# Performance work log

Hardware: AMD Instinct MI355X
Metric: run time of the kernel (lower is better)

Reference implementation:

```python
import jax, jax.numpy as jnp
import numpy as np

# Analytic closed form of the 4-qubit circuit. Wires (0,1) and (2,3) are
# independent 2-qubit blocks: RY(x_a)oRY(x_b) -> CNOT(a,b) -> RY(p_a)oRY(p_b).
# Heisenberg picture gives:
#   <Z_a> = cos(p_a)*cos(x_a) + sin(p_a)*sin(x_a)*sin(x_b)
#   <Z_b> = cos(p_b)*cos(x_a)*cos(x_b) + sin(p_b)*sin(x_b)

def setup_inputs() -> dict:
    key = jax.random.key(0)
    k1, k2, k3, k4 = jax.random.split(key, 4)
    B = 16384
    return {
        "x": jax.random.uniform(k1, (B, 1, 28, 28), dtype=jnp.float32),
        "vqc_params": jax.random.normal(k2, (4,), dtype=jnp.float32),
        "fc_w": jax.random.normal(k3, (10, 784), dtype=jnp.float32) * 0.05,
        "fc_b": jax.random.normal(k4, (10,), dtype=jnp.float32) * 0.05,
        "bias": jnp.zeros((10,), dtype=jnp.float32),
    }


def _pair_expvals(xa, xb, pa, pb):
    # xa, xb: [B, 196]; pa, pb: scalars
    za = jnp.cos(pa) * jnp.cos(xa) + jnp.sin(pa) * jnp.sin(xa) * jnp.sin(xb)
    zb = jnp.cos(pb) * jnp.cos(xa) * jnp.cos(xb) + jnp.sin(pb) * jnp.sin(xb)
    return za, zb


def reference(x, vqc_params, fc_w, fc_b, bias):
    B = x.shape[0]
    # Extract 2x2 patches in the same (r, c) row-major order as the torch loop.
    # [B,28,28] -> [B,14,2,14,2] -> [B,14,14,2,2] -> [B,196,4]
    p = x[:, 0].reshape(B, 14, 2, 14, 2).transpose(0, 1, 3, 2, 4).reshape(B, 196, 4)
    x0, x1, x2, x3 = p[..., 0], p[..., 1], p[..., 2], p[..., 3]
    p0, p1, p2, p3 = vqc_params[0], vqc_params[1], vqc_params[2], vqc_params[3]
    z0, z1 = _pair_expvals(x0, x1, p0, p1)
    z2, z3 = _pair_expvals(x2, x3, p2, p3)
    q = jnp.stack([z0, z1, z2, z3], axis=-1).reshape(B, 4 * 196)  # patch-major, wire-minor
    logits = q @ fc_w.T + fc_b - bias
    return jax.nn.log_softmax(logits, axis=-1)
```

## Files before the change

kernel.cpp:

```cpp
#include <hip/hip_runtime.h>


typedef __attribute__((ext_vector_type(8))) short short8;
typedef __attribute__((ext_vector_type(4))) float f32x4;

constexpr int WAVES = 4;
constexpr int BLOCK = WAVES * 64;
constexpr int IMGS  = 16;
constexpr int NITER = 7;
constexpr int S2    = 800;

static __device__ __forceinline__ unsigned pkbf2(float lo, float hi) {
    unsigned r;
    asm("v_cvt_pk_bf16_f32 %0, %1, %2" : "=v"(r) : "v"(lo), "v"(hi));
    return r;
}

__global__ __launch_bounds__(BLOCK, 4)
void quanv_mfma(const float* __restrict__ x,
                const float* __restrict__ vqc,
                const float* __restrict__ fc_w,
                const float* __restrict__ fc_b,
                const float* __restrict__ bias,
                float* __restrict__ out,
                int B)
{
    __shared__ __align__(16) unsigned short q_lds[IMGS * S2];
    __shared__ float cpart[3][64 * 4];

    const int tid  = threadIdx.x;
    const int lane = tid & 63;
    const int wv   = tid >> 6;
    const int i16  = lane & 15;
    const int g    = lane >> 4;
    const int imgBase = blockIdx.x * IMGS;

    float S0, C0, S1, C1, S2p, C2p, S3, C3;
    __sincosf(vqc[0], &S0, &C0);
    __sincosf(vqc[1], &S1, &C1);
    __sincosf(vqc[2], &S2p, &C2p);
    __sincosf(vqc[3], &S3, &C3);

    const float4* __restrict__ xf4 =
        reinterpret_cast<const float4*>(x) + (long)imgBase * 196;
    #pragma unroll
    for (int it = 0; it < 13; ++it) {
        const unsigned u = it * BLOCK + tid;
        if (it < 12 || u < 3136u) {
            const float4 v = xf4[u];
            const unsigned img = u / 196u;
            const unsigned jv  = u - 196u * img;
            const unsigned y   = jv / 7u;
            const unsigned cx  = jv - 7u * y;
            const unsigned par = y & 1u;

            const float CA = par ? C2p : C0, SA = par ? S2p : S0;
            const float CB = par ? C3  : C1, SB = par ? S3  : S1;

            float sa, ca, sb, cb;
            __sincosf(v.x, &sa, &ca);  __sincosf(v.y, &sb, &cb);
            const float za1 = CA * ca + SA * (sa * sb);
            const float zb1 = CB * (ca * cb) + SB * sb;
            __sincosf(v.z, &sa, &ca);  __sincosf(v.w, &sb, &cb);
            const float za2 = CA * ca + SA * (sa * sb);
            const float zb2 = CB * (ca * cb) + SB * sb;

            const unsigned qb = ((y >> 1) * 14u + 2u * cx) * 4u + 2u * par;
            const unsigned e  = img * S2 + qb;
            *reinterpret_cast<unsigned*>(&q_lds[e])     = pkbf2(za1, zb1);
            *reinterpret_cast<unsigned*>(&q_lds[e + 4]) = pkbf2(za2, zb2);
        }
    }
    if (tid < 128) {
        const int img = tid >> 3, o = (tid & 7) << 1;
        *reinterpret_cast<unsigned*>(&q_lds[img * S2 + 784 + o]) = 0u;
    }

    const int ncl = (i16 < 10) ? i16 : 9;
    const float* __restrict__ wrow = fc_w + ncl * 784;
    short8 bf[NITER];
    #pragma unroll
    for (int I = 0; I < NITER; ++I) {
        int kb = wv + 4 * I; if (kb > 24) kb = 24;
        int k  = kb * 32 + 8 * g; if (k > 776) k = 776;
        const float4 lo4 = *reinterpret_cast<const float4*>(wrow + k);
        const float4 hi4 = *reinterpret_cast<const float4*>(wrow + k + 4);
        union { unsigned u[4]; short8 s; } t;
        t.u[0] = pkbf2(lo4.x, lo4.y);
        t.u[1] = pkbf2(lo4.z, lo4.w);
        t.u[2] = pkbf2(hi4.x, hi4.y);
        t.u[3] = pkbf2(hi4.z, hi4.w);
        bf[I] = t.s;
    }

    __syncthreads();

    f32x4 acc = {0.f, 0.f, 0.f, 0.f};
    #pragma unroll
    for (int I = 0; I < NITER; ++I) {
        const int kb = wv + 4 * I;
        if (kb < 25) {
            const short8 a = *reinterpret_cast<const short8*>(
                &q_lds[i16 * S2 + kb * 32 + 8 * g]);
            acc = __builtin_amdgcn_mfma_f32_16x16x32_bf16(a, bf[I], acc, 0, 0, 0);
        }
    }

    if (wv > 0)
        *reinterpret_cast<f32x4*>(&cpart[wv - 1][lane * 4]) = acc;
    __syncthreads();

    if (wv == 0) {
        #pragma unroll
        for (int p = 0; p < 3; ++p)
            acc += *reinterpret_cast<const f32x4*>(&cpart[p][lane * 4]);
        const float bk = (i16 < 10) ? (fc_b[i16] - bias[i16]) : 0.f;

        #pragma unroll
        for (int r = 0; r < 4; ++r) {
            const float lg = acc[r] + bk;
            float mx = (i16 < 10) ? lg : -3.0e38f;
            #pragma unroll
            for (int off = 1; off < 16; off <<= 1)
                mx = fmaxf(mx, __shfl_xor(mx, off, 64));
            float s = (i16 < 10) ? __expf(lg - mx) : 0.f;
            #pragma unroll
            for (int off = 1; off < 16; off <<= 1)
                s += __shfl_xor(s, off, 64);
            const int im = imgBase + g * 4 + r;
            if (i16 < 10 && im < B)
                out[(long)im * 10 + i16] = lg - mx - __logf(s);
        }
    }
}

extern "C" void kernel_launch(void* const* d_in, const int* in_sizes, int n_in,
                              void* d_out, int out_size, void* d_ws, size_t ws_size,
                              hipStream_t stream) {
    const float* x    = (const float*)d_in[0];
    const float* vqc  = (const float*)d_in[1];
    const float* fc_w = (const float*)d_in[2];
    const float* fc_b = (const float*)d_in[3];
    const float* bias = (const float*)d_in[4];
    float* outp = (float*)d_out;

    const int B = in_sizes[0] / 784;
    const int nblocks = (B + IMGS - 1) / IMGS;
    hipLaunchKernelGGL(quanv_mfma, dim3(nblocks), dim3(BLOCK), 0, stream,
                       x, vqc, fc_w, fc_b, bias, outp, B);
}
```

Baseline: 17.99 us.

## Use 512-thread blocks with 8-wave K split and incremental patch indexing

Doubles the block to 8 waves, so the load/sincos phase runs in about 7 iterations per thread and the MFMA K loop splits 8 ways instead of 4. Image/patch indices now advance incrementally and use a multiply-shift divide. The cross-wave reduction buffer reuses the q LDS region behind an extra barrier, and the LDS row stride is padded to 808. Weight loads move after the first barrier, and the final reduction sums seven partials in wave 0.

Measured after the change: 17.61 us. 1.02x faster.

```diff
diff --git a/kernel.cpp b/kernel.cpp
--- a/kernel.cpp
+++ b/kernel.cpp
@@ -4,11 +4,10 @@
 typedef __attribute__((ext_vector_type(8))) short short8;
 typedef __attribute__((ext_vector_type(4))) float f32x4;
 
-constexpr int WAVES = 4;
-constexpr int BLOCK = WAVES * 64;
+constexpr int BLOCK = 512;
 constexpr int IMGS  = 16;
-constexpr int NITER = 7;
-constexpr int S2    = 800;
+constexpr int S2    = 808;
+constexpr int NIT   = 4;
 
 static __device__ __forceinline__ unsigned pkbf2(float lo, float hi) {
     unsigned r;
@@ -16,7 +15,7 @@
     return r;
 }
 
-__global__ __launch_bounds__(BLOCK, 4)
+__global__ __launch_bounds__(BLOCK, 6)
 void quanv_mfma(const float* __restrict__ x,
                 const float* __restrict__ vqc,
                 const float* __restrict__ fc_w,
@@ -26,7 +25,6 @@
                 int B)
 {
     __shared__ __align__(16) unsigned short q_lds[IMGS * S2];
-    __shared__ float cpart[3][64 * 4];
 
     const int tid  = threadIdx.x;
     const int lane = tid & 63;
@@ -41,64 +39,79 @@
     __sincosf(vqc[2], &S2p, &C2p);
     __sincosf(vqc[3], &S3, &C3);
 
+    if (tid < 192) {
+        const unsigned im = (unsigned)tid / 12u;
+        const unsigned o  = (unsigned)tid - 12u * im;
+        *reinterpret_cast<unsigned*>(&q_lds[im * S2 + 784 + 2 * o]) = 0u;
+    }
+
     const float4* __restrict__ xf4 =
         reinterpret_cast<const float4*>(x) + (long)imgBase * 196;
+
+    unsigned img = (unsigned)tid / 196u;
+    unsigned jv  = (unsigned)tid - 196u * img;
+
+    auto process = [&](float4 v, unsigned im, unsigned j) {
+        const unsigned y   = (j * 1171u) >> 13;
+        const unsigned cx  = j - 7u * y;
+        const unsigned par = y & 1u;
+        const float CA = par ? C2p : C0, SA = par ? S2p : S0;
+        const float CB = par ? C3  : C1, SB = par ? S3  : S1;
+        float sa, ca, sb, cb;
+        __sincosf(v.x, &sa, &ca);  __sincosf(v.y, &sb, &cb);
+        const float za1 = CA * ca + SA * (sa * sb);
+        const float zb1 = CB * (ca * cb) + SB * sb;
+        __sincosf(v.z, &sa, &ca);  __sincosf(v.w, &sb, &cb);
+        const float za2 = CA * ca + SA * (sa * sb);
+        const float zb2 = CB * (ca * cb) + SB * sb;
+        const unsigned e = im * S2 + (y >> 1) * 56u + 8u * cx + 2u * par;
+        *reinterpret_cast<unsigned*>(&q_lds[e])     = pkbf2(za1, zb1);
+        *reinterpret_cast<unsigned*>(&q_lds[e + 4]) = pkbf2(za2, zb2);
+    };
+
     #pragma unroll
-    for (int it = 0; it < 13; ++it) {
-        const unsigned u = it * BLOCK + tid;
-        if (it < 12 || u < 3136u) {
-            const float4 v = xf4[u];
-            const unsigned img = u / 196u;
-            const unsigned jv  = u - 196u * img;
-            const unsigned y   = jv / 7u;
-            const unsigned cx  = jv - 7u * y;
-            const unsigned par = y & 1u;
-
-            const float CA = par ? C2p : C0, SA = par ? S2p : S0;
-            const float CB = par ? C3  : C1, SB = par ? S3  : S1;
-
-            float sa, ca, sb, cb;
-            __sincosf(v.x, &sa, &ca);  __sincosf(v.y, &sb, &cb);
-            const float za1 = CA * ca + SA * (sa * sb);
-            const float zb1 = CB * (ca * cb) + SB * sb;
-            __sincosf(v.z, &sa, &ca);  __sincosf(v.w, &sb, &cb);
-            const float za2 = CA * ca + SA * (sa * sb);
-            const float zb2 = CB * (ca * cb) + SB * sb;
-
-            const unsigned qb = ((y >> 1) * 14u + 2u * cx) * 4u + 2u * par;
-            const unsigned e  = img * S2 + qb;
-            *reinterpret_cast<unsigned*>(&q_lds[e])     = pkbf2(za1, zb1);
-            *reinterpret_cast<unsigned*>(&q_lds[e + 4]) = pkbf2(za2, zb2);
-        }
+    for (int bt = 0; bt < 2; ++bt) {
+        const float4 r0 = xf4[(bt * 3 + 0) * BLOCK + tid];
+        const float4 r1 = xf4[(bt * 3 + 1) * BLOCK + tid];
+        const float4 r2 = xf4[(bt * 3 + 2) * BLOCK + tid];
+        process(r0, img, jv);
+        img += 2; jv += 120; if (jv >= 196) { jv -= 196; img += 1; }
+        process(r1, img, jv);
+        img += 2; jv += 120; if (jv >= 196) { jv -= 196; img += 1; }
+        process(r2, img, jv);
+        img += 2; jv += 120; if (jv >= 196) { jv -= 196; img += 1; }
     }
-    if (tid < 128) {
-        const int img = tid >> 3, o = (tid & 7) << 1;
-        *reinterpret_cast<unsigned*>(&q_lds[img * S2 + 784 + o]) = 0u;
-    }
-
-    const int ncl = (i16 < 10) ? i16 : 9;
-    const float* __restrict__ wrow = fc_w + ncl * 784;
-    short8 bf[NITER];
-    #pragma unroll
-    for (int I = 0; I < NITER; ++I) {
-        int kb = wv + 4 * I; if (kb > 24) kb = 24;
-        int k  = kb * 32 + 8 * g; if (k > 776) k = 776;
-        const float4 lo4 = *reinterpret_cast<const float4*>(wrow + k);
-        const float4 hi4 = *reinterpret_cast<const float4*>(wrow + k + 4);
-        union { unsigned u[4]; short8 s; } t;
-        t.u[0] = pkbf2(lo4.x, lo4.y);
-        t.u[1] = pkbf2(lo4.z, lo4.w);
-        t.u[2] = pkbf2(hi4.x, hi4.y);
-        t.u[3] = pkbf2(hi4.z, hi4.w);
-        bf[I] = t.s;
+    if (tid < 64) {
+        const float4 r = xf4[6 * BLOCK + tid];
+        process(r, img, jv);
     }
 
     __syncthreads();
 
+    const int ncl = (i16 < 10) ? i16 : 9;
+    const float* __restrict__ wrow = fc_w + ncl * 784;
+    short8 bf[NIT];
+    #pragma unroll
+    for (int I = 0; I < NIT; ++I) {
+        const int kb = wv + 8 * I;
+        if (kb < 25) {
+            int k = kb * 32 + 8 * g;
+            if (k > 776) k = 776;
+            const float4 lo4 = *reinterpret_cast<const float4*>(wrow + k);
+            const float4 hi4 = *reinterpret_cast<const float4*>(wrow + k + 4);
+            union { unsigned u[4]; short8 s; } t;
+            t.u[0] = pkbf2(lo4.x, lo4.y);
+            t.u[1] = pkbf2(lo4.z, lo4.w);
+            t.u[2] = pkbf2(hi4.x, hi4.y);
+            t.u[3] = pkbf2(hi4.z, hi4.w);
+            bf[I] = t.s;
+        }
+    }
+
     f32x4 acc = {0.f, 0.f, 0.f, 0.f};
     #pragma unroll
-    for (int I = 0; I < NITER; ++I) {
-        const int kb = wv + 4 * I;
+    for (int I = 0; I < NIT; ++I) {
+        const int kb = wv + 8 * I;
         if (kb < 25) {
             const short8 a = *reinterpret_cast<const short8*>(
                 &q_lds[i16 * S2 + kb * 32 + 8 * g]);
@@ -106,14 +119,16 @@
         }
     }
 
+    __syncthreads();
+    float* const cpart = reinterpret_cast<float*>(q_lds);
     if (wv > 0)
-        *reinterpret_cast<f32x4*>(&cpart[wv - 1][lane * 4]) = acc;
+        *reinterpret_cast<f32x4*>(&cpart[(wv - 1) * 256 + lane * 4]) = acc;
     __syncthreads();
 
     if (wv == 0) {
         #pragma unroll
-        for (int p = 0; p < 3; ++p)
-            acc += *reinterpret_cast<const f32x4*>(&cpart[p][lane * 4]);
+        for (int p = 0; p < 7; ++p)
+            acc += *reinterpret_cast<const f32x4*>(&cpart[p * 256 + lane * 4]);
         const float bk = (i16 < 10) ? (fc_b[i16] - bias[i16]) : 0.f;
 
         #pragma unroll
```
